# Optimization experiments

Hardware: AMD Instinct MI355X
Metric: run time of the kernel (lower is better)

## Reference

```python
import jax, jax.numpy as jnp
import numpy as np

B, S, D, H, HD, WIN = 2, 2048, 2048, 16, 128, 1024
EPS = 1e-06
SCALE = HD ** -0.5


def rotate_half(x):
    x1 = x[..., : x.shape[-1] // 2]
    x2 = x[..., x.shape[-1] // 2 :]
    return jnp.concatenate((-x2, x1), axis=-1)


def setup_inputs() -> dict:
    key = jax.random.key(0)
    ks = jax.random.split(key, 6)
    hidden_states = jax.random.normal(ks[0], (B, S, D), jnp.float32)
    # RoPE tables (HF-style: freqs duplicated across the two halves)
    pos = jnp.arange(S, dtype=jnp.float32)
    inv_freq = 1.0 / (10000.0 ** (jnp.arange(0, HD, 2, dtype=jnp.float32) / HD))
    freqs = pos[:, None] * inv_freq[None, :]            # [S, HD/2]
    emb = jnp.concatenate([freqs, freqs], axis=-1)      # [S, HD]
    cos = jnp.broadcast_to(jnp.cos(emb)[None], (B, S, HD)).astype(jnp.float32)
    sin = jnp.broadcast_to(jnp.sin(emb)[None], (B, S, HD)).astype(jnp.float32)
    std = 1.0 / np.sqrt(D)
    Wq = jax.random.normal(ks[1], (D, H * HD), jnp.float32) * std
    Wk = jax.random.normal(ks[2], (D, H * HD), jnp.float32) * std
    Wv = jax.random.normal(ks[3], (D, H * HD), jnp.float32) * std
    Wo = jax.random.normal(ks[4], (H * HD, D), jnp.float32) * (1.0 / np.sqrt(H * HD))
    q_scale = jnp.ones((HD,), jnp.float32)
    k_scale = jnp.ones((HD,), jnp.float32)
    return {"hidden_states": hidden_states, "cos": cos, "sin": sin,
            "Wq": Wq, "Wk": Wk, "Wv": Wv, "Wo": Wo,
            "q_scale": q_scale, "k_scale": k_scale}


def _rmsnorm(x, scale):
    var = jnp.mean(x * x, axis=-1, keepdims=True)
    return scale * (x * jax.lax.rsqrt(var + EPS))


def reference(hidden_states, cos, sin, Wq, Wk, Wv, Wo, q_scale, k_scale):
    b, s, _ = hidden_states.shape
    q = (hidden_states @ Wq).reshape(b, s, H, HD)
    k = (hidden_states @ Wk).reshape(b, s, H, HD)
    v = (hidden_states @ Wv).reshape(b, s, H, HD)
    q = _rmsnorm(q, q_scale)
    k = _rmsnorm(k, k_scale)
    # RoPE, unsqueeze_dim=2 (head axis)
    c = cos[:, :, None, :]
    sn = sin[:, :, None, :]
    q = q * c + rotate_half(q) * sn
    k = k * c + rotate_half(k) * sn
    scores = jnp.einsum("bqhd,bkhd->bhqk", q, k) * SCALE  # [B,H,S,S]
    i = jnp.arange(s)[:, None]
    j = jnp.arange(s)[None, :]
    mask = (j <= i) & (j >= i - WIN)  # causal + sliding window
    scores = jnp.where(mask[None, None], scores, jnp.finfo(scores.dtype).min)
    probs = jax.nn.softmax(scores, axis=-1)
    out = jnp.einsum("bhqk,bkhd->bqhd", probs, v).reshape(b, s, H * HD)
    return out @ Wo
```

## Files before the change

kernel.cpp:

```cpp
#include <hip/hip_runtime.h>

#define B_ 2
#define S_ 2048
#define D_ 2048
#define H_ 16
#define HD_ 128
#define WIN_ 1024
#define M_ (B_*S_)
#define N_ (H_*HD_)
#define SCALE_ 0.08838834764831845f
#define CSHIFT_ 11.5f

typedef unsigned short u16;
typedef __attribute__((ext_vector_type(8))) short short8;
typedef __attribute__((ext_vector_type(4))) float f32x4;

__device__ __forceinline__ float b2f(u16 u) {
    union { unsigned int i; float f; } x; x.i = ((unsigned int)u) << 16; return x.f;
}
__device__ __forceinline__ u16 f2b(float f) {
    union { float f; unsigned int i; } x; x.f = f;
    unsigned int u = x.i;
    return (u16)((u + 0x7fffu + ((u >> 16) & 1u)) >> 16);
}

__device__ __forceinline__ void async_ld16(const u16* g, u16* l) {
    __builtin_amdgcn_global_load_lds(
        (const __attribute__((address_space(1))) unsigned int*)g,
        (__attribute__((address_space(3))) unsigned int*)l, 16, 0, 0);
}

__global__ __launch_bounds__(256) void cvt_kernel(const float* __restrict__ in,
                                                  u16* __restrict__ out, int n4) {
    int i = blockIdx.x * 256 + threadIdx.x;
    if (i >= n4) return;
    float4 v = ((const float4*)in)[i];
    ushort4 o;
    o.x = f2b(v.x); o.y = f2b(v.y); o.z = f2b(v.z); o.w = f2b(v.w);
    ((ushort4*)out)[i] = o;
}

__global__ __launch_bounds__(256) void transpose4_kernel(const float* __restrict__ W0, const float* __restrict__ W1,
                                                         const float* __restrict__ W2, const float* __restrict__ W3,
                                                         u16* __restrict__ O0, u16* __restrict__ O1,
                                                         u16* __restrict__ O2, u16* __restrict__ O3) {
    __shared__ float tile[32][33];
    const float* in; u16* out;
    switch (blockIdx.z) {
        case 0: in = W0; out = O0; break;
        case 1: in = W1; out = O1; break;
        case 2: in = W2; out = O2; break;
        default: in = W3; out = O3; break;
    }
    const int C = 2048, R = 2048;
    int c0 = blockIdx.x * 32, r0 = blockIdx.y * 32;
    int tx = threadIdx.x & 31, ty = threadIdx.x >> 5;
#pragma unroll
    for (int rr = ty; rr < 32; rr += 8)
        tile[rr][tx] = in[(long)(r0 + rr) * C + c0 + tx];
    __syncthreads();
#pragma unroll
    for (int cc = ty; cc < 32; cc += 8)
        out[(long)(c0 + cc) * R + r0 + tx] = f2b(tile[tx][cc]);
}


__global__ __launch_bounds__(256) void gemm_qkv_kernel(const u16* __restrict__ A,
                                                       const u16* __restrict__ Bt3,
                                                       u16* __restrict__ Qb,
                                                       u16* __restrict__ Kb,
                                                       u16* __restrict__ Vtb) {
    constexpr int Kk = 2048;
    __shared__ u16 As[128 * 32];
    __shared__ u16 Bs[128 * 32];

    const int tid  = threadIdx.x;
    const int m0   = blockIdx.y * 128, n0 = blockIdx.x * 128;
    const int wid  = tid >> 6, lane = tid & 63;
    const int wm   = (wid >> 1) * 64, wn = (wid & 1) * 64;
    const int quad = lane >> 4, lrow = lane & 15;
    const int lr4  = lane >> 2, lc8 = (lane & 3) * 8;

    f32x4 acc[4][4];
#pragma unroll
    for (int a = 0; a < 4; ++a)
#pragma unroll
        for (int b = 0; b < 4; ++b) acc[a][b] = (f32x4)0.0f;

    for (int k0 = 0; k0 < Kk; k0 += 32) {
        __syncthreads();
#pragma unroll
        for (int it = 0; it < 2; ++it) {
            const int ra = (wid + 4 * it) * 16;
            async_ld16(&A  [(long)(m0 + ra + lr4) * Kk + k0 + lc8], &As[ra * 32]);
            async_ld16(&Bt3[(long)(n0 + ra + lr4) * Kk + k0 + lc8], &Bs[ra * 32]);
        }
        __syncthreads();

        short8 af[4], bf[4];
#pragma unroll
        for (int t = 0; t < 4; ++t)
            af[t] = *(const short8*)&As[(wm + t * 16 + lrow) * 32 + quad * 8];
#pragma unroll
        for (int t = 0; t < 4; ++t)
            bf[t] = *(const short8*)&Bs[(wn + t * 16 + lrow) * 32 + quad * 8];
#pragma unroll
        for (int tm = 0; tm < 4; ++tm)
#pragma unroll
            for (int tn = 0; tn < 4; ++tn)
                acc[tm][tn] = __builtin_amdgcn_mfma_f32_16x16x32_bf16(
                    af[tm], bf[tn], acc[tm][tn], 0, 0, 0);
    }

    const int seg = n0 >> 11;
#pragma unroll
    for (int tm = 0; tm < 4; ++tm)
#pragma unroll
        for (int tn = 0; tn < 4; ++tn) {
            const int colg = (n0 & 2047) + wn + tn * 16 + lrow;
            const int rowb = m0 + wm + tm * 16 + quad * 4;
            if (seg == 2) {
                const int b = rowb >> 11, s = rowb & (S_ - 1);
                const int h = colg >> 7, d = colg & (HD_ - 1);
                ushort4 pk;
                pk.x = f2b(acc[tm][tn][0]); pk.y = f2b(acc[tm][tn][1]);
                pk.z = f2b(acc[tm][tn][2]); pk.w = f2b(acc[tm][tn][3]);
                *(ushort4*)&Vtb[((long)((b * H_ + h) * HD_ + d)) * S_ + s] = pk;
            } else {
                u16* dst = (seg == 0) ? Qb : Kb;
#pragma unroll
                for (int r = 0; r < 4; ++r)
                    dst[(long)(rowb + r) * N_ + colg] = f2b(acc[tm][tn][r]);
            }
        }
}

__global__ __launch_bounds__(256) void gemm_out_kernel(const u16* __restrict__ A,
                                                       const u16* __restrict__ Bt,
                                                       float* __restrict__ C) {
    constexpr int Kk = 2048, Nn = 2048;
    __shared__ u16 As[128 * 32];
    __shared__ u16 Bs[128 * 32];

    const int tid  = threadIdx.x;
    const int m0   = blockIdx.y * 128, n0 = blockIdx.x * 128;
    const int wid  = tid >> 6, lane = tid & 63;
    const int wm   = (wid >> 1) * 64, wn = (wid & 1) * 64;
    const int quad = lane >> 4, lrow = lane & 15;
    const int lr4  = lane >> 2, lc8 = (lane & 3) * 8;

    f32x4 acc[4][4];
#pragma unroll
    for (int a = 0; a < 4; ++a)
#pragma unroll
        for (int b = 0; b < 4; ++b) acc[a][b] = (f32x4)0.0f;

    for (int k0 = 0; k0 < Kk; k0 += 32) {
        __syncthreads();
#pragma unroll
        for (int it = 0; it < 2; ++it) {
            const int ra = (wid + 4 * it) * 16;
            async_ld16(&A [(long)(m0 + ra + lr4) * Kk + k0 + lc8], &As[ra * 32]);
            async_ld16(&Bt[(long)(n0 + ra + lr4) * Kk + k0 + lc8], &Bs[ra * 32]);
        }
        __syncthreads();

        short8 af[4], bf[4];
#pragma unroll
        for (int t = 0; t < 4; ++t)
            af[t] = *(const short8*)&As[(wm + t * 16 + lrow) * 32 + quad * 8];
#pragma unroll
        for (int t = 0; t < 4; ++t)
            bf[t] = *(const short8*)&Bs[(wn + t * 16 + lrow) * 32 + quad * 8];
#pragma unroll
        for (int tm = 0; tm < 4; ++tm)
#pragma unroll
            for (int tn = 0; tn < 4; ++tn)
                acc[tm][tn] = __builtin_amdgcn_mfma_f32_16x16x32_bf16(
                    af[tm], bf[tn], acc[tm][tn], 0, 0, 0);
    }

#pragma unroll
    for (int tm = 0; tm < 4; ++tm)
#pragma unroll
        for (int tn = 0; tn < 4; ++tn) {
            const int col  = n0 + wn + tn * 16 + lrow;
            const int rowb = m0 + wm + tm * 16 + quad * 4;
#pragma unroll
            for (int r = 0; r < 4; ++r)
                C[(long)(rowb + r) * Nn + col] = acc[tm][tn][r];
        }
}

__global__ __launch_bounds__(256) void norm_rope_kernel(u16* __restrict__ X,
                                                        const float* __restrict__ scale,
                                                        const float* __restrict__ cosp,
                                                        const float* __restrict__ sinp) {
    int wid = threadIdx.x >> 6, lane = threadIdx.x & 63;
    int row = blockIdx.x * 4 + wid;
    int bs  = row >> 4;
    long off = (long)row * HD_;
    float x1 = b2f(X[off + lane]);
    float x2 = b2f(X[off + lane + 64]);
    float ss = x1 * x1 + x2 * x2;
#pragma unroll
    for (int o = 1; o < 64; o <<= 1) ss += __shfl_xor(ss, o);
    float inv = rsqrtf(ss * (1.0f / HD_) + 1e-6f);
    long cb = (long)bs * HD_;
    float c1 = cosp[cb + lane],      s1 = sinp[cb + lane];
    float c2 = cosp[cb + lane + 64], s2 = sinp[cb + lane + 64];
    float n1 = scale[lane] * x1 * inv;
    float n2 = scale[lane + 64] * x2 * inv;
    X[off + lane]      = f2b(n1 * c1 - n2 * s1);
    X[off + lane + 64] = f2b(n2 * c2 + n1 * s2);
}

__global__ __launch_bounds__(512, 4) void fattn_kernel(const u16* __restrict__ Q,
                                                       const u16* __restrict__ K,
                                                       const u16* __restrict__ Vt,
                                                       u16* __restrict__ O) {
    __shared__ u16 Ks[64 * 128];
    __shared__ u16 Vs[128 * 64];
    __shared__ u16 Ps[8][16 * 72];

    const int tid  = threadIdx.x;
    const int wid  = tid >> 6, lane = tid & 63;
    const int quad = lane >> 4, lrow = lane & 15;
    const int qb = 15 - (blockIdx.x & 15);
    const int h  = (blockIdx.x >> 4) & (H_ - 1);
    const int b  = blockIdx.x >> 8;
    const int q0  = qb * 128;
    const int q0w = q0 + wid * 16;

    short8 qf[4];
    const long qrow = ((long)(b * S_ + q0w + lrow) * H_ + h) * HD_;
#pragma unroll
    for (int c = 0; c < 4; ++c)
        qf[c] = *(const short8*)&Q[qrow + c * 32 + quad * 8];

    float l_r[4] = {0.f, 0.f, 0.f, 0.f};
    f32x4 oacc[8];
#pragma unroll
    for (int t = 0; t < 8; ++t) oacc[t] = (f32x4)0.0f;

    const int ktlo = (q0 - WIN_ > 0) ? (q0 - WIN_) : 0;
    const long kgbase = ((long)b * S_ * H_ + h) * HD_;
    const long vgbase = ((long)(b * H_ + h) * HD_) * S_;
    const int lxor = lrow & 7;

    for (int kt0 = ktlo; kt0 < q0 + 128; kt0 += 64) {
        __syncthreads();
#pragma unroll
        for (int it = 0; it < 2; ++it) {
            const int rb = (wid * 2 + it) * 4;
            const int row = rb + (lane >> 4);
            const int cg = (lane & 15) ^ (row & 7);
            async_ld16(&K[kgbase + (long)(kt0 + row) * (H_ * HD_) + cg * 8], &Ks[rb * 128]);
        }
#pragma unroll
        for (int it = 0; it < 2; ++it) {
            const int db = (wid * 2 + it) * 8;
            const int d = db + (lane >> 3);
            const int cg = (lane & 7) ^ (d & 7);
            async_ld16(&Vt[vgbase + (long)d * S_ + kt0 + cg * 8], &Vs[db * 64]);
        }
        __syncthreads();

        const bool active = (kt0 <= q0w + 15) && (kt0 + 63 >= q0w - WIN_);
        if (active) {
            f32x4 cs[4];
#pragma unroll
            for (int t = 0; t < 4; ++t) {
                cs[t] = (f32x4)0.0f;
                const int krow = (t * 16 + lrow) * 128;
#pragma unroll
                for (int c = 0; c < 4; ++c) {
                    short8 kf = *(const short8*)&Ks[krow + (((c * 4 + quad) ^ lxor) * 8)];
                    cs[t] = __builtin_amdgcn_mfma_f32_16x16x32_bf16(qf[c], kf, cs[t], 0, 0, 0);
                }
            }

            const bool full = (kt0 + 63 <= q0w) && (kt0 >= q0w + 15 - WIN_);
            if (!full) {
#pragma unroll
                for (int t = 0; t < 4; ++t) {
                    const int jc = kt0 + t * 16 + lrow;
#pragma unroll
                    for (int r = 0; r < 4; ++r) {
                        const int i = q0w + quad * 4 + r;
                        if (jc > i || jc < i - WIN_) cs[t][r] = -1e30f;
                    }
                }
            }

#pragma unroll
            for (int t = 0; t < 4; ++t)
#pragma unroll
                for (int r = 0; r < 4; ++r) {
                    float p = __expf(fmaf(cs[t][r], SCALE_, -CSHIFT_));
                    l_r[r] += p;
                    Ps[wid][(quad * 4 + r) * 72 + t * 16 + lrow] = f2b(p);
                }

            short8 pf0 = *(const short8*)&Ps[wid][lrow * 72 + quad * 8];
            short8 pf1 = *(const short8*)&Ps[wid][lrow * 72 + 32 + quad * 8];
#pragma unroll
            for (int t = 0; t < 8; ++t) {
                const int vrow = (t * 16 + lrow) * 64;
                short8 vf0 = *(const short8*)&Vs[vrow + ((quad ^ lxor) * 8)];
                short8 vf1 = *(const short8*)&Vs[vrow + (((quad + 4) ^ lxor) * 8)];
                oacc[t] = __builtin_amdgcn_mfma_f32_16x16x32_bf16(pf0, vf0, oacc[t], 0, 0, 0);
                oacc[t] = __builtin_amdgcn_mfma_f32_16x16x32_bf16(pf1, vf1, oacc[t], 0, 0, 0);
            }
        }
    }

    float inv[4];
#pragma unroll
    for (int r = 0; r < 4; ++r) {
        float v = l_r[r];
#pragma unroll
        for (int o = 1; o < 16; o <<= 1) v += __shfl_xor(v, o);
        inv[r] = 1.0f / v;
    }

#pragma unroll
    for (int t = 0; t < 8; ++t) {
        const int d = t * 16 + lrow;
#pragma unroll
        for (int r = 0; r < 4; ++r) {
            const int q = q0w + quad * 4 + r;
            O[(long)(b * S_ + q) * N_ + h * HD_ + d] = f2b(oacc[t][r] * inv[r]);
        }
    }
}

extern "C" void kernel_launch(void* const* d_in, const int* in_sizes, int n_in,
                              void* d_out, int out_size, void* d_ws, size_t ws_size,
                              hipStream_t stream) {
    const float* hs   = (const float*)d_in[0];
    const float* cosp = (const float*)d_in[1];
    const float* sinp = (const float*)d_in[2];
    const float* Wq   = (const float*)d_in[3];
    const float* Wk   = (const float*)d_in[4];
    const float* Wv   = (const float*)d_in[5];
    const float* Wo   = (const float*)d_in[6];
    const float* qsc  = (const float*)d_in[7];
    const float* ksc  = (const float*)d_in[8];
    float* out = (float*)d_out;

    char* ws = (char*)d_ws;
    const size_t MD = (size_t)M_ * D_;
    const size_t WN = (size_t)D_ * N_;
    u16* hsb = (u16*)ws;
    u16* Wqt = (u16*)(ws + MD * 2);
    u16* Wkt = Wqt + WN;
    u16* Wvt = Wkt + WN;
    u16* Wot = Wvt + WN;
    u16* Qb  = Wot + WN;
    u16* Kb  = Qb + MD;
    u16* Vtb = Kb + MD;
    u16* Ab  = hsb;

    cvt_kernel<<<(int)(MD / 4 / 256), 256, 0, stream>>>(hs, hsb, (int)(MD / 4));
    dim3 tg(64, 64, 4);
    transpose4_kernel<<<tg, 256, 0, stream>>>(Wq, Wk, Wv, Wo, Wqt, Wkt, Wvt, Wot);

    dim3 gqkv(48, 32);
    gemm_qkv_kernel<<<gqkv, 256, 0, stream>>>(hsb, Wqt, Qb, Kb, Vtb);

    norm_rope_kernel<<<B_ * S_ * H_ / 4, 256, 0, stream>>>(Qb, qsc, cosp, sinp);
    norm_rope_kernel<<<B_ * S_ * H_ / 4, 256, 0, stream>>>(Kb, ksc, cosp, sinp);

    fattn_kernel<<<B_ * H_ * (S_ / 128), 512, 0, stream>>>(Qb, Kb, Vtb, Ab);

    dim3 gout(16, 32);
    gemm_out_kernel<<<gout, 256, 0, stream>>>(Ab, Wot, out);
}
```

Before: 421.3 us.

## Fuse RMSNorm and RoPE into QKV GEMM epilogue and swizzle LDS tiles

Removes the two separate norm_rope launches by computing the per-head sum of squares, the scale, and the rotate-half RoPE inside the QKV GEMM epilogue. Partial sums and half-rows are exchanged through shared memory. This avoids a global round trip of Q and K in bf16. The epilogue also rounds to bf16 only once instead of twice. Separately, both GEMMs now XOR-swizzle the 16-byte chunks in their LDS tiles to reduce bank conflicts, at the cost of more shared memory and extra barriers in the epilogue.

After: 425.9 us. About the same (+1.1%).

```diff
diff --git a/kernel.cpp b/kernel.cpp
--- a/kernel.cpp
+++ b/kernel.cpp
@@ -64,22 +64,30 @@
         out[(long)(c0 + cc) * R + r0 + tx] = f2b(tile[tx][cc]);
 }
 
-
 __global__ __launch_bounds__(256) void gemm_qkv_kernel(const u16* __restrict__ A,
                                                        const u16* __restrict__ Bt3,
                                                        u16* __restrict__ Qb,
                                                        u16* __restrict__ Kb,
-                                                       u16* __restrict__ Vtb) {
+                                                       u16* __restrict__ Vtb,
+                                                       const float* __restrict__ qsc,
+                                                       const float* __restrict__ ksc,
+                                                       const float* __restrict__ cosp,
+                                                       const float* __restrict__ sinp) {
     constexpr int Kk = 2048;
-    __shared__ u16 As[128 * 32];
-    __shared__ u16 Bs[128 * 32];
+    __shared__ char smem[34816];
+    u16* As = (u16*)smem;
+    u16* Bs = (u16*)(smem + 8192);
+    float* ssq  = (float*)smem;
+    float* xbuf = (float*)(smem + 1024);
 
     const int tid  = threadIdx.x;
     const int m0   = blockIdx.y * 128, n0 = blockIdx.x * 128;
     const int wid  = tid >> 6, lane = tid & 63;
     const int wm   = (wid >> 1) * 64, wn = (wid & 1) * 64;
     const int quad = lane >> 4, lrow = lane & 15;
-    const int lr4  = lane >> 2, lc8 = (lane & 3) * 8;
+    const int lr4  = lane >> 2, lc4 = lane & 3;
+    const int swz  = (lr4 >> 1) & 3;
+    const int rsw  = (lrow >> 1) & 3;
 
     f32x4 acc[4][4];
 #pragma unroll
@@ -92,18 +100,18 @@
 #pragma unroll
         for (int it = 0; it < 2; ++it) {
             const int ra = (wid + 4 * it) * 16;
-            async_ld16(&A  [(long)(m0 + ra + lr4) * Kk + k0 + lc8], &As[ra * 32]);
-            async_ld16(&Bt3[(long)(n0 + ra + lr4) * Kk + k0 + lc8], &Bs[ra * 32]);
+            async_ld16(&A  [(long)(m0 + ra + lr4) * Kk + k0 + ((lc4 ^ swz) * 8)], &As[ra * 32]);
+            async_ld16(&Bt3[(long)(n0 + ra + lr4) * Kk + k0 + ((lc4 ^ swz) * 8)], &Bs[ra * 32]);
         }
         __syncthreads();
 
         short8 af[4], bf[4];
 #pragma unroll
         for (int t = 0; t < 4; ++t)
-            af[t] = *(const short8*)&As[(wm + t * 16 + lrow) * 32 + quad * 8];
+            af[t] = *(const short8*)&As[(wm + t * 16 + lrow) * 32 + ((quad ^ rsw) * 8)];
 #pragma unroll
         for (int t = 0; t < 4; ++t)
-            bf[t] = *(const short8*)&Bs[(wn + t * 16 + lrow) * 32 + quad * 8];
+            bf[t] = *(const short8*)&Bs[(wn + t * 16 + lrow) * 32 + ((quad ^ rsw) * 8)];
 #pragma unroll
         for (int tm = 0; tm < 4; ++tm)
 #pragma unroll
@@ -113,26 +121,114 @@
     }
 
     const int seg = n0 >> 11;
-#pragma unroll
-    for (int tm = 0; tm < 4; ++tm)
-#pragma unroll
-        for (int tn = 0; tn < 4; ++tn) {
-            const int colg = (n0 & 2047) + wn + tn * 16 + lrow;
-            const int rowb = m0 + wm + tm * 16 + quad * 4;
-            if (seg == 2) {
+    if (seg == 2) {
+#pragma unroll
+        for (int tm = 0; tm < 4; ++tm)
+#pragma unroll
+            for (int tn = 0; tn < 4; ++tn) {
+                const int colg = (n0 & 2047) + wn + tn * 16 + lrow;
+                const int rowb = m0 + wm + tm * 16 + quad * 4;
                 const int b = rowb >> 11, s = rowb & (S_ - 1);
                 const int h = colg >> 7, d = colg & (HD_ - 1);
                 ushort4 pk;
                 pk.x = f2b(acc[tm][tn][0]); pk.y = f2b(acc[tm][tn][1]);
                 pk.z = f2b(acc[tm][tn][2]); pk.w = f2b(acc[tm][tn][3]);
                 *(ushort4*)&Vtb[((long)((b * H_ + h) * HD_ + d)) * S_ + s] = pk;
-            } else {
-                u16* dst = (seg == 0) ? Qb : Kb;
+            }
+        return;
+    }
+
+    __syncthreads();
+
+    float ss[4][4];
+#pragma unroll
+    for (int tm = 0; tm < 4; ++tm)
+#pragma unroll
+        for (int r = 0; r < 4; ++r) {
+            float v = acc[tm][0][r] * acc[tm][0][r] + acc[tm][1][r] * acc[tm][1][r]
+                    + acc[tm][2][r] * acc[tm][2][r] + acc[tm][3][r] * acc[tm][3][r];
+#pragma unroll
+            for (int o = 1; o < 16; o <<= 1) v += __shfl_xor(v, o);
+            ss[tm][r] = v;
+        }
+    if (lrow == 0) {
+#pragma unroll
+        for (int tm = 0; tm < 4; ++tm)
+#pragma unroll
+            for (int r = 0; r < 4; ++r)
+                ssq[(wn >> 6) * 128 + wm + tm * 16 + quad * 4 + r] = ss[tm][r];
+    }
+    __syncthreads();
+
+    const float* scp = (seg == 0) ? qsc : ksc;
+    float sc[4];
+#pragma unroll
+    for (int tn = 0; tn < 4; ++tn) sc[tn] = scp[wn + tn * 16 + lrow];
+#pragma unroll
+    for (int tm = 0; tm < 4; ++tm)
+#pragma unroll
+        for (int r = 0; r < 4; ++r) {
+            const int row = wm + tm * 16 + quad * 4 + r;
+            const float inv = rsqrtf((ssq[row] + ssq[128 + row]) * (1.0f / HD_) + 1e-6f);
+#pragma unroll
+            for (int tn = 0; tn < 4; ++tn) acc[tm][tn][r] *= sc[tn] * inv;
+        }
+
+    u16* dst = (seg == 0) ? Qb : Kb;
+    const bool hi = (wn != 0);
+
+    if (hi) {
+#pragma unroll
+        for (int tm = 0; tm < 4; ++tm)
+#pragma unroll
+            for (int tn = 0; tn < 4; ++tn)
 #pragma unroll
                 for (int r = 0; r < 4; ++r)
-                    dst[(long)(rowb + r) * N_ + colg] = f2b(acc[tm][tn][r]);
-            }
-        }
+                    xbuf[(wm + tm * 16 + quad * 4 + r) * 66 + tn * 16 + lrow] = acc[tm][tn][r];
+    }
+    __syncthreads();
+    if (!hi) {
+#pragma unroll
+        for (int tm = 0; tm < 4; ++tm)
+#pragma unroll
+            for (int tn = 0; tn < 4; ++tn) {
+                const int d = tn * 16 + lrow;
+#pragma unroll
+                for (int r = 0; r < 4; ++r) {
+                    const int rowl = wm + tm * 16 + quad * 4 + r;
+                    const int tok  = m0 + rowl;
+                    const long cb  = (long)(tok & (S_ - 1)) * HD_ + d;
+                    const float p  = xbuf[rowl * 66 + d];
+                    const float v  = acc[tm][tn][r] * cosp[cb] - p * sinp[cb];
+                    dst[(long)tok * N_ + (n0 & 2047) + d] = f2b(v);
+                }
+            }
+#pragma unroll
+        for (int tm = 0; tm < 4; ++tm)
+#pragma unroll
+            for (int tn = 0; tn < 4; ++tn)
+#pragma unroll
+                for (int r = 0; r < 4; ++r)
+                    xbuf[(wm + tm * 16 + quad * 4 + r) * 66 + tn * 16 + lrow] = acc[tm][tn][r];
+    }
+    __syncthreads();
+    if (hi) {
+#pragma unroll
+        for (int tm = 0; tm < 4; ++tm)
+#pragma unroll
+            for (int tn = 0; tn < 4; ++tn) {
+                const int dl = tn * 16 + lrow;
+#pragma unroll
+                for (int r = 0; r < 4; ++r) {
+                    const int rowl = wm + tm * 16 + quad * 4 + r;
+                    const int tok  = m0 + rowl;
+                    const long cb  = (long)(tok & (S_ - 1)) * HD_ + 64 + dl;
+                    const float p  = xbuf[rowl * 66 + dl];
+                    const float v  = acc[tm][tn][r] * cosp[cb] + p * sinp[cb];
+                    dst[(long)tok * N_ + (n0 & 2047) + 64 + dl] = f2b(v);
+                }
+            }
+    }
 }
 
 __global__ __launch_bounds__(256) void gemm_out_kernel(const u16* __restrict__ A,
@@ -147,7 +243,9 @@
     const int wid  = tid >> 6, lane = tid & 63;
     const int wm   = (wid >> 1) * 64, wn = (wid & 1) * 64;
     const int quad = lane >> 4, lrow = lane & 15;
-    const int lr4  = lane >> 2, lc8 = (lane & 3) * 8;
+    const int lr4  = lane >> 2, lc4 = lane & 3;
+    const int swz  = (lr4 >> 1) & 3;
+    const int rsw  = (lrow >> 1) & 3;
 
     f32x4 acc[4][4];
 #pragma unroll
@@ -160,18 +258,18 @@
 #pragma unroll
         for (int it = 0; it < 2; ++it) {
             const int ra = (wid + 4 * it) * 16;
-            async_ld16(&A [(long)(m0 + ra + lr4) * Kk + k0 + lc8], &As[ra * 32]);
-            async_ld16(&Bt[(long)(n0 + ra + lr4) * Kk + k0 + lc8], &Bs[ra * 32]);
+            async_ld16(&A [(long)(m0 + ra + lr4) * Kk + k0 + ((lc4 ^ swz) * 8)], &As[ra * 32]);
+            async_ld16(&Bt[(long)(n0 + ra + lr4) * Kk + k0 + ((lc4 ^ swz) * 8)], &Bs[ra * 32]);
         }
         __syncthreads();
 
         short8 af[4], bf[4];
 #pragma unroll
         for (int t = 0; t < 4; ++t)
-            af[t] = *(const short8*)&As[(wm + t * 16 + lrow) * 32 + quad * 8];
+            af[t] = *(const short8*)&As[(wm + t * 16 + lrow) * 32 + ((quad ^ rsw) * 8)];
 #pragma unroll
         for (int t = 0; t < 4; ++t)
-            bf[t] = *(const short8*)&Bs[(wn + t * 16 + lrow) * 32 + quad * 8];
+            bf[t] = *(const short8*)&Bs[(wn + t * 16 + lrow) * 32 + ((quad ^ rsw) * 8)];
 #pragma unroll
         for (int tm = 0; tm < 4; ++tm)
 #pragma unroll
@@ -190,29 +288,6 @@
             for (int r = 0; r < 4; ++r)
                 C[(long)(rowb + r) * Nn + col] = acc[tm][tn][r];
         }
-}
-
-__global__ __launch_bounds__(256) void norm_rope_kernel(u16* __restrict__ X,
-                                                        const float* __restrict__ scale,
-                                                        const float* __restrict__ cosp,
-                                                        const float* __restrict__ sinp) {
-    int wid = threadIdx.x >> 6, lane = threadIdx.x & 63;
-    int row = blockIdx.x * 4 + wid;
-    int bs  = row >> 4;
-    long off = (long)row * HD_;
-    float x1 = b2f(X[off + lane]);
-    float x2 = b2f(X[off + lane + 64]);
-    float ss = x1 * x1 + x2 * x2;
-#pragma unroll
-    for (int o = 1; o < 64; o <<= 1) ss += __shfl_xor(ss, o);
-    float inv = rsqrtf(ss * (1.0f / HD_) + 1e-6f);
-    long cb = (long)bs * HD_;
-    float c1 = cosp[cb + lane],      s1 = sinp[cb + lane];
-    float c2 = cosp[cb + lane + 64], s2 = sinp[cb + lane + 64];
-    float n1 = scale[lane] * x1 * inv;
-    float n2 = scale[lane + 64] * x2 * inv;
-    X[off + lane]      = f2b(n1 * c1 - n2 * s1);
-    X[off + lane + 64] = f2b(n2 * c2 + n1 * s2);
 }
 
 __global__ __launch_bounds__(512, 4) void fattn_kernel(const u16* __restrict__ Q,
@@ -367,10 +442,7 @@
     transpose4_kernel<<<tg, 256, 0, stream>>>(Wq, Wk, Wv, Wo, Wqt, Wkt, Wvt, Wot);
 
     dim3 gqkv(48, 32);
-    gemm_qkv_kernel<<<gqkv, 256, 0, stream>>>(hsb, Wqt, Qb, Kb, Vtb);
-
-    norm_rope_kernel<<<B_ * S_ * H_ / 4, 256, 0, stream>>>(Qb, qsc, cosp, sinp);
-    norm_rope_kernel<<<B_ * S_ * H_ / 4, 256, 0, stream>>>(Kb, ksc, cosp, sinp);
+    gemm_qkv_kernel<<<gqkv, 256, 0, stream>>>(hsb, Wqt, Qb, Kb, Vtb, qsc, ksc, cosp, sinp);
 
     fattn_kernel<<<B_ * H_ * (S_ / 128), 512, 0, stream>>>(Qb, Kb, Vtb, Ab);
 
```
